# Kernel tuning notes

Hardware: AMD Instinct MI355X
Metric: run time of the kernel (lower is better)

The kernel has to match this reference:

```python
import jax, jax.numpy as jnp
import numpy as np

N_NODES = 100_000
N_EDGES = 1_600_000
N_GRAPHS = 512
HID = 64
NUM_CLASSES = 100
VOCAB = 3100
ID_OFFSET = 1500
BN_EPS = 1e-5


def setup_inputs() -> dict:
    key = jax.random.key(0)
    ks = jax.random.split(key, 8)
    node_ids = jax.random.randint(ks[0], (N_NODES,), 0, 1600)
    edge_src = jax.random.randint(ks[1], (N_EDGES,), 0, N_NODES)
    edge_dst = jax.random.randint(ks[2], (N_EDGES,), 0, N_NODES)
    graph_ids = jnp.sort(jax.random.randint(ks[3], (N_NODES,), 0, N_GRAPHS))
    emb = jax.random.normal(ks[4], (VOCAB, HID), dtype=jnp.float32) * 0.02
    # 3 GIN layers x 3 MLP linear layers, all 64->64 since embedding_dim == hidden
    Ws = jax.random.normal(ks[5], (3, 3, HID, HID), dtype=jnp.float32) * 0.05
    bs = jnp.zeros((3, 3, HID), dtype=jnp.float32)
    bn_gamma = jnp.ones((3, HID), dtype=jnp.float32)
    bn_beta = jnp.zeros((3, HID), dtype=jnp.float32)
    eps = jnp.zeros((3,), dtype=jnp.float32)  # learn_eps=True, init 0
    W_out = jax.random.normal(ks[6], (3 * HID, NUM_CLASSES), dtype=jnp.float32) * 0.05
    b_out = jnp.zeros((NUM_CLASSES,), dtype=jnp.float32)
    return {"node_ids": node_ids, "edge_src": edge_src, "edge_dst": edge_dst,
            "graph_ids": graph_ids, "emb": emb, "Ws": Ws, "bs": bs,
            "bn_gamma": bn_gamma, "bn_beta": bn_beta, "eps": eps,
            "W_out": W_out, "b_out": b_out}


def reference(node_ids, edge_src, edge_dst, graph_ids, emb, Ws, bs,
              bn_gamma, bn_beta, eps, W_out, b_out):
    n = node_ids.shape[0]
    h = emb[node_ids + ID_OFFSET]  # [N, HID]
    pooled = []
    for l in range(3):  # GIN layers (fixed small count)
        # GINConv, sum aggregator: (1+eps)*h + sum over in-edges of h[src]
        agg = jax.ops.segment_sum(h[edge_src], edge_dst, num_segments=n)
        x = (1.0 + eps[l]) * h + agg
        for m in range(3):
            x = jax.nn.relu(x @ Ws[l, m] + bs[l, m])
        mean = x.mean(axis=0)
        var = x.var(axis=0)  # biased var, as torch BN uses for normalization
        x = (x - mean) * jax.lax.rsqrt(var + BN_EPS) * bn_gamma[l] + bn_beta[l]
        h = x
        # dgl.sum_nodes: per-graph segment sum
        pooled.append(jax.ops.segment_sum(h, graph_ids, num_segments=N_GRAPHS))
    graph_features = jnp.concatenate(pooled, axis=-1)  # [G, 3*HID]
    return graph_features @ W_out + b_out  # [G, NUM_CLASSES]
```

## Files before the change

kernel.cpp:

```cpp
#include <hip/hip_runtime.h>

#define N_NODES 100000
#define N_EDGES 1600000
#define N_GRAPHS 512
#define HID 64
#define NUM_CLASSES 100
#define ID_OFFSET 1500
#define BN_EPS 1e-5f
#define CAP 64
#define NBKT 256
#define BSHIFT 9
#define NUSED ((N_NODES + 511) >> 9)
#define BCAP 10240
#define CBLK 98
#define CHUNK 16384
#define WPBLK 5
#define EMBBLK ((N_NODES * 32 + 1023) / 1024)
#define ZWORDS (98304 + 3072 + 100000)
#define ZBLK ((ZWORDS + 1023) / 1024)
#define DUMMY_ROW 100000
#define SREP 8
#define SSTRIDE 384

typedef __attribute__((ext_vector_type(8))) short short8;
typedef __attribute__((ext_vector_type(4))) float floatx4;

__device__ __forceinline__ float b2f(unsigned short u) {
    return __builtin_bit_cast(float, ((unsigned)u) << 16);
}
__device__ __forceinline__ unsigned short f2b(float f) {
    unsigned x = __builtin_bit_cast(unsigned, f);
    x += 0x7FFFu + ((x >> 16) & 1u);
    return (unsigned short)(x >> 16);
}

#define XSH(row, qq) ((((((row) >> 4) << 7) + ((qq) << 4) + (((row) & 15) ^ (qq))) * 8))


__global__ __launch_bounds__(1024) void prep_kernel(const int* __restrict__ src,
                                                    const int* __restrict__ dst,
                                                    int* __restrict__ cursor,
                                                    int* __restrict__ rec,
                                                    const float* __restrict__ Ws,
                                                    unsigned short* __restrict__ whi,
                                                    unsigned short* __restrict__ wlo,
                                                    const int* __restrict__ node_ids,
                                                    const int* __restrict__ gid,
                                                    const float* __restrict__ emb,
                                                    unsigned short* __restrict__ h,
                                                    unsigned short* __restrict__ xin,
                                                    int* __restrict__ gs,
                                                    int* __restrict__ ge,
                                                    unsigned* __restrict__ zbase) {
    __shared__ int hist[NBKT];
    __shared__ int base_s[NBKT];
    int t = threadIdx.x;
    int blk = blockIdx.x;

    if (blk < CBLK) {
        if (blk == 0 && t < 32) {
            ((unsigned*)(h + (size_t)DUMMY_ROW * 64))[t] = 0u;
            ((unsigned*)(xin + (size_t)DUMMY_ROW * 64))[t] = 0u;
        }
        if (t < NBKT) hist[t] = 0;
        __syncthreads();
        int cb = blk * CHUNK;
        int d_[16], s_[16];
#pragma unroll
        for (int k = 0; k < 16; ++k) {
            int i = cb + k * 1024 + t;
            d_[k] = (i < N_EDGES) ? dst[i] : -1;
            s_[k] = (i < N_EDGES) ? src[i] : 0;
            if (d_[k] >= 0) atomicAdd(&hist[((unsigned)d_[k] >> BSHIFT) & (NBKT - 1)], 1);
        }
        __syncthreads();
        if (t < NBKT) base_s[t] = (hist[t] > 0) ? atomicAdd(&cursor[t], hist[t]) : 0;
        __syncthreads();
        if (t < NBKT) hist[t] = 0;
        __syncthreads();
#pragma unroll
        for (int k = 0; k < 16; ++k) {
            if (d_[k] >= 0) {
                unsigned d = (unsigned)d_[k];
                int b = (d >> BSHIFT) & (NBKT - 1);
                int p = atomicAdd(&hist[b], 1);
                int g = base_s[b] + p;
                if ((unsigned)g < BCAP)
                    rec[b * BCAP + g] = ((int)(d & 511) << 17) | (s_[k] & 0x1FFFF);
            }
        }
    } else if (blk < CBLK + WPBLK) {
        int G = (blk - CBLK) * 1024 + t;
        if (G < 3 * 1536) {
            int l = G / 1536, Gp = G % 1536;
            int mm = Gp >> 9, rem = Gp & 511;
            int kq = rem >> 6, n = rem & 63;
            const float* Wp = Ws + l * 12288 + mm * 4096 + (kq * 8) * 64 + n;
            unsigned short uh[8], ul[8];
#pragma unroll
            for (int j = 0; j < 8; ++j) {
                float w = Wp[j * 64];
                unsigned short hi = f2b(w);
                uh[j] = hi;
                ul[j] = f2b(w - b2f(hi));
            }
            size_t off = (size_t)l * 12288 + (mm << 12) + XSH(n, kq);
            *(short8*)&whi[off] = *(short8*)uh;
            *(short8*)&wlo[off] = *(short8*)ul;
        }
    } else if (blk < CBLK + WPBLK + EMBBLK) {
        int idx = (blk - CBLK - WPBLK) * 1024 + t;
        if (idx < N_NODES * 32) {
            int n = idx >> 5, cp = idx & 31;
            const float2 e = *(const float2*)(emb + (((size_t)(node_ids[n] + ID_OFFSET)) << 6) + cp * 2);
            unsigned v = (unsigned)f2b(e.x) | ((unsigned)f2b(e.y) << 16);
            ((unsigned*)h)[n * 32 + cp] = v;
            if (cp == 0) {
                int g = gid[n] & (N_GRAPHS - 1);
                if (n == 0 || (gid[n - 1] & (N_GRAPHS - 1)) != g) gs[g] = n;
                if (n == N_NODES - 1 || (gid[n + 1] & (N_GRAPHS - 1)) != g) ge[g] = n + 1;
            }
        }
    } else {
        int idx = (blk - CBLK - WPBLK - EMBBLK) * 1024 + t;
        if (idx < ZWORDS) zbase[idx] = 0u;
    }
}


__global__ __launch_bounds__(1024) void fill_kernel(const int* __restrict__ rec,
                                                    const int* __restrict__ cursor,
                                                    int* __restrict__ cnt,
                                                    int* __restrict__ srcs) {
    __shared__ int lcnt[512];
    int t = threadIdx.x;
    int b = blockIdx.x;
    if (t < 512) lcnt[t] = 0;
    __syncthreads();
    int nb = cursor[b];
    if (nb < 0) nb = 0;
    if (nb > BCAP) nb = BCAP;
    const int* seg = rec + b * BCAP;
    for (int i = t; i < nb; i += 1024) {
        unsigned r = (unsigned)seg[i];
        int dl = (int)((r >> 17) & 511);
        int s = (int)(r & 0x1FFFF);
        int node = (b << BSHIFT) + dl;
        int p = atomicAdd(&lcnt[dl], 1);
        if (p < CAP && node < N_NODES) srcs[(node << 6) + p] = s;
    }
    __syncthreads();
    if (t < 512) {
        int node = (b << BSHIFT) + t;
        if (node < N_NODES) cnt[node] = lcnt[t];
    }
    __syncthreads();
    for (int i = t; i < 512 * 64; i += 1024) {
        int nl = i >> 6, p = i & 63;
        int node = (b << BSHIFT) + nl;
        if (node < N_NODES) {
            int deg = lcnt[nl];
            int degc = deg > CAP ? CAP : deg;
            int degp = (degc + 15) & ~15;
            if (degp < 16) degp = 16;
            if (p >= degc && p < degp) srcs[(node << 6) + p] = DUMMY_ROW;
        }
    }
}


__global__ __launch_bounds__(256) void agg_kernel(const unsigned short* __restrict__ x,
                                                  const int* __restrict__ cnt,
                                                  const int* __restrict__ srcs,
                                                  const float* __restrict__ eps, int l,
                                                  const float* __restrict__ stats,
                                                  const float* __restrict__ gamma,
                                                  const float* __restrict__ beta,
                                                  unsigned short* __restrict__ out) {
    int nb = __builtin_amdgcn_readfirstlane(((blockIdx.x << 2) + (threadIdx.x >> 6)) << 2);
    int lane = threadIdx.x & 63;
    int half = lane >> 5;
    int cl = lane & 31;
    const unsigned* __restrict__ xu = (const unsigned*)x;

    float scale = 1.0f + eps[l];
    float a0f = 1.0f, a1f = 1.0f, b0f = 0.0f, b1f = 0.0f;
    if (l > 0) {
        int lp = l - 1;
        float sm0 = 0.f, sm1 = 0.f, sq0 = 0.f, sq1 = 0.f;
#pragma unroll
        for (int rp = 0; rp < SREP; ++rp) {
            const float* sp = stats + rp * SSTRIDE + lp * 128;
            float2 a_ = *(const float2*)&sp[2 * cl];
            float2 b_ = *(const float2*)&sp[64 + 2 * cl];
            sm0 += a_.x; sm1 += a_.y;
            sq0 += b_.x; sq1 += b_.y;
        }
        float2 gm = *(const float2*)&gamma[lp * 64 + 2 * cl];
        float2 bt = *(const float2*)&beta[lp * 64 + 2 * cl];
        float mean0 = sm0 * (1.0f / N_NODES);
        float var0 = sq0 * (1.0f / N_NODES) - mean0 * mean0;
        float r0 = rsqrtf(var0 + BN_EPS);
        a0f = gm.x * r0;
        b0f = bt.x - mean0 * a0f;
        float mean1 = sm1 * (1.0f / N_NODES);
        float var1 = sq1 * (1.0f / N_NODES) - mean1 * mean1;
        float r1 = rsqrtf(var1 + BN_EPS);
        a1f = gm.y * r1;
        b1f = bt.y - mean1 * a1f;
    }

    int deg[4], degp[4];
    const int* row[4];
#pragma unroll
    for (int n = 0; n < 4; ++n) {
        int d = cnt[nb + n];
        int dc = d < 0 ? 0 : (d > CAP ? CAP : d);
        deg[n] = dc;
        int dp = (dc + 15) & ~15;
        degp[n] = dp < 16 ? 16 : dp;
        row[n] = srcs + ((size_t)(nb + n) << 6);
    }
    int cmax = degp[0];
    cmax = degp[1] > cmax ? degp[1] : cmax;
    cmax = degp[2] > cmax ? degp[2] : cmax;
    cmax = degp[3] > cmax ? degp[3] : cmax;

    unsigned us[4];
#pragma unroll
    for (int n = 0; n < 4; ++n) us[n] = xu[(size_t)(nb + n) * 32 + cl];

    float A0[4] = {0.f, 0.f, 0.f, 0.f}, A1[4] = {0.f, 0.f, 0.f, 0.f};
    float B0[4] = {0.f, 0.f, 0.f, 0.f}, B1[4] = {0.f, 0.f, 0.f, 0.f};

    {
        unsigned uv[4][8];
#pragma unroll
        for (int n = 0; n < 4; ++n)
#pragma unroll
            for (int k = 0; k < 8; ++k) {
                int ia = row[n][2 * k] & 0x1FFFF;
                int ib = row[n][2 * k + 1] & 0x1FFFF;
                int idx = half ? ib : ia;
                uv[n][k] = xu[(size_t)idx * 32 + cl];
            }
#pragma unroll
        for (int n = 0; n < 4; ++n)
#pragma unroll
            for (int k = 0; k < 8; ++k) {
                float lo = b2f((unsigned short)(uv[n][k] & 0xFFFF));
                float hi = b2f((unsigned short)(uv[n][k] >> 16));
                if (k & 1) { B0[n] += lo; B1[n] += hi; }
                else       { A0[n] += lo; A1[n] += hi; }
            }
    }

    for (int c = 16; c < cmax; c += 16) {
        unsigned uc[4][8];
#pragma unroll
        for (int n = 0; n < 4; ++n)
            if (c < degp[n])
#pragma unroll
                for (int k = 0; k < 8; ++k) {
                    int ia = row[n][c + 2 * k] & 0x1FFFF;
                    int ib = row[n][c + 2 * k + 1] & 0x1FFFF;
                    int idx = half ? ib : ia;
                    uc[n][k] = xu[(size_t)idx * 32 + cl];
                }
#pragma unroll
        for (int n = 0; n < 4; ++n)
            if (c < degp[n])
#pragma unroll
                for (int k = 0; k < 8; ++k) {
                    float lo = b2f((unsigned short)(uc[n][k] & 0xFFFF));
                    float hi = b2f((unsigned short)(uc[n][k] >> 16));
                    if (k & 1) { B0[n] += lo; B1[n] += hi; }
                    else       { A0[n] += lo; A1[n] += hi; }
                }
    }

#pragma unroll
    for (int n = 0; n < 4; ++n) {
        float S0 = (A0[n] + B0[n]);
        float S1 = (A1[n] + B1[n]);
        S0 += __shfl_xor(S0, 32);
        S1 += __shfl_xor(S1, 32);
        if (half == 0) {
            float selflo = b2f((unsigned short)(us[n] & 0xFFFF));
            float selfhi = b2f((unsigned short)(us[n] >> 16));
            float db = scale + (float)deg[n];
            float v0 = fmaf(a0f, fmaf(scale, selflo, S0), db * b0f);
            float v1 = fmaf(a1f, fmaf(scale, selfhi, S1), db * b1f);
            ((unsigned*)out)[(size_t)(nb + n) * 32 + cl] =
                (unsigned)f2b(v0) | ((unsigned)f2b(v1) << 16);
        }
    }
}


__global__ __launch_bounds__(256, 4) void mlp_kernel(unsigned short* __restrict__ x,
                                                     const unsigned short* __restrict__ whi,
                                                     const unsigned short* __restrict__ wlo,
                                                     const float* __restrict__ bs, int l,
                                                     float* __restrict__ stats,
                                                     const int* __restrict__ graph_ids,
                                                     float* __restrict__ pooled, int last) {
    __shared__ __align__(16) unsigned short xs[64 * 64];
    __shared__ int garr[64];
    __shared__ float ssum[256], sqq[256];
    int t = threadIdx.x;
    int nodebase = blockIdx.x * 64;
    int lane = t & 63, w = t >> 6;
    int m = lane & 15, q = lane >> 4;

    const unsigned short* xrow = x + (((size_t)(nodebase + w * 16 + m)) << 6);
    short8 a0[2];
#pragma unroll
    for (int kc = 0; kc < 2; ++kc)
        a0[kc] = *(const short8*)&xrow[kc * 32 + q * 8];

    if (lane < 16) {
        int n = nodebase + w * 16 + lane;
        garr[w * 16 + lane] = (n < N_NODES) ? (graph_ids[n] & (N_GRAPHS - 1)) : -1;
    }

    const float* bb = bs + l * 3 * 64;
    const unsigned short* whil = whi + (size_t)l * 12288;
    const unsigned short* wlol = wlo + (size_t)l * 12288;
    for (int mm = 0; mm < 3; ++mm) {
        short8 bl[2][4];
#pragma unroll
        for (int kc = 0; kc < 2; ++kc)
#pragma unroll
            for (int tj = 0; tj < 4; ++tj)
                bl[kc][tj] = *(const short8*)&wlol[(mm << 12) + XSH(tj * 16 + m, kc * 4 + q)];
        short8 a[2];
        if (mm == 0) {
#pragma unroll
            for (int kc = 0; kc < 2; ++kc) a[kc] = a0[kc];
        } else {
#pragma unroll
            for (int kc = 0; kc < 2; ++kc)
                a[kc] = *(const short8*)&xs[XSH(w * 16 + m, kc * 4 + q)];
        }

        floatx4 acc[4];
#pragma unroll
        for (int tj = 0; tj < 4; ++tj) {
            float bv = bb[mm * 64 + tj * 16 + m];
            acc[tj] = (floatx4){bv, bv, bv, bv};
        }
#pragma unroll
        for (int kc = 0; kc < 2; ++kc) {
            short8 bh[4];
#pragma unroll
            for (int tj = 0; tj < 4; ++tj)
                bh[tj] = *(const short8*)&whil[(mm << 12) + XSH(tj * 16 + m, kc * 4 + q)];
#pragma unroll
            for (int tj = 0; tj < 4; ++tj)
                acc[tj] = __builtin_amdgcn_mfma_f32_16x16x32_bf16(a[kc], bh[tj], acc[tj], 0, 0, 0);
        }
#pragma unroll
        for (int kc = 0; kc < 2; ++kc)
#pragma unroll
            for (int tj = 0; tj < 4; ++tj)
                acc[tj] = __builtin_amdgcn_mfma_f32_16x16x32_bf16(a[kc], bl[kc][tj], acc[tj], 0, 0, 0);
#pragma unroll
        for (int tj = 0; tj < 4; ++tj) {
            int col = tj * 16 + m;
#pragma unroll
            for (int r = 0; r < 4; ++r) {
                int row = w * 16 + q * 4 + r;
                float v = acc[tj][r];
                xs[XSH(row, col >> 3) + (col & 7)] = f2b(v > 0.f ? v : 0.f);
            }
        }
    }

    if (!last) {
        unsigned* xo = (unsigned*)x;
#pragma unroll
        for (int it = 0; it < 8; ++it) {
            int row = w * 16 + (lane >> 5) + it * 2;
            int cp = lane & 31;
            int col = cp * 2;
            unsigned val = *(const unsigned*)&xs[XSH(row, col >> 3) + (col & 7)];
            int node = nodebase + row;
            if (node < N_NODES) xo[(size_t)node * 32 + cp] = val;
        }
    }
    {
        int c = lane;
        float s = 0.f, q2 = 0.f, acc2 = 0.f;
        int cur = -1;
#pragma unroll
        for (int k = 0; k < 16; ++k) {
            int row = w * 16 + k;
            int g = garr[row];
            if (g >= 0) {
                float v = b2f(xs[XSH(row, c >> 3) + (c & 7)]);
                s += v;
                q2 += v * v;
                if (g != cur) {
                    if (cur >= 0) atomicAdd(&pooled[cur * 192 + l * 64 + c], acc2);
                    acc2 = 0.f;
                    cur = g;
                }
                acc2 += v;
            }
        }
        if (cur >= 0) atomicAdd(&pooled[cur * 192 + l * 64 + c], acc2);
        ssum[t] = s;
        sqq[t] = q2;
    }
    __syncthreads();
    if (t < 64) {
        float S = ssum[t] + ssum[t + 64] + ssum[t + 128] + ssum[t + 192];
        float Q = sqq[t] + sqq[t + 64] + sqq[t + 128] + sqq[t + 192];
        float* sp = stats + (blockIdx.x & (SREP - 1)) * SSTRIDE + l * 128;
        atomicAdd(&sp[t], S);
        atomicAdd(&sp[64 + t], Q);
    }
}


__global__ __launch_bounds__(256) void out_kernel(const float* __restrict__ pooled,
                                                  const float* __restrict__ stats,
                                                  const float* __restrict__ gamma,
                                                  const float* __restrict__ beta,
                                                  const int* __restrict__ gs,
                                                  const int* __restrict__ ge,
                                                  const float* __restrict__ Wo,
                                                  const float* __restrict__ bo,
                                                  float* __restrict__ out) {
    __shared__ float sab[384];
    int t = threadIdx.x;
    if (t < 192) {
        int l2 = t / 64, c = t & 63;
        float S = 0.f, Q = 0.f;
#pragma unroll
        for (int rp = 0; rp < SREP; ++rp) {
            S += stats[rp * SSTRIDE + l2 * 128 + c];
            Q += stats[rp * SSTRIDE + l2 * 128 + 64 + c];
        }
        float mean = S * (1.0f / N_NODES);
        float var = Q * (1.0f / N_NODES) - mean * mean;
        float rstd = rsqrtf(var + BN_EPS);
        float a = gamma[l2 * 64 + c] * rstd;
        sab[l2 * 128 + c] = a;
        sab[l2 * 128 + 64 + c] = beta[l2 * 64 + c] - mean * a;
    }
    __syncthreads();
    int idx = blockIdx.x * blockDim.x + t;
    if (idx < N_GRAPHS * NUM_CLASSES) {
        int g = idx / NUM_CLASSES, k = idx % NUM_CLASSES;
        float cg = (float)(ge[g] - gs[g]);
        float acc = bo[k];
        for (int l2 = 0; l2 < 3; ++l2)
            for (int c = 0; c < 64; ++c) {
                float gf = fmaf(sab[l2 * 128 + c], pooled[g * 192 + l2 * 64 + c],
                                sab[l2 * 128 + 64 + c] * cg);
                acc = fmaf(gf, Wo[(l2 * 64 + c) * NUM_CLASSES + k], acc);
            }
        out[idx] = acc;
    }
}

extern "C" void kernel_launch(void* const* d_in, const int* in_sizes, int n_in,
                              void* d_out, int out_size, void* d_ws, size_t ws_size,
                              hipStream_t stream) {
    const int*   node_ids  = (const int*)d_in[0];
    const int*   edge_src  = (const int*)d_in[1];
    const int*   edge_dst  = (const int*)d_in[2];
    const int*   graph_ids = (const int*)d_in[3];
    const float* emb       = (const float*)d_in[4];
    const float* Ws        = (const float*)d_in[5];
    const float* bs        = (const float*)d_in[6];
    const float* gamma     = (const float*)d_in[7];
    const float* beta      = (const float*)d_in[8];
    const float* eps       = (const float*)d_in[9];
    const float* W_out     = (const float*)d_in[10];
    const float* b_out     = (const float*)d_in[11];
    float* out = (float*)d_out;

    unsigned short* h    = (unsigned short*)d_ws;
    unsigned short* xin  = h + 6400000 + 8192;
    unsigned short* whi  = xin + 6400000 + 8192;
    unsigned short* wlo  = whi + 36864;
    int*   srcs   = (int*)(wlo + 36864);
    int*   rec    = srcs + 6400000;
    float* pooled = (float*)(rec + NUSED * BCAP);
    float* stats  = pooled + 98304;
    int*   cnt    = (int*)(stats + SREP * SSTRIDE);
    int*   gs     = cnt + 100000;
    int*   ge     = gs + 512;
    int*   cursor = ge + 512;

    hipMemsetAsync(gs, 0, (size_t)(512 + 512 + 256) * 4, stream);

    prep_kernel<<<CBLK + WPBLK + EMBBLK + ZBLK, 1024, 0, stream>>>(
        edge_src, edge_dst, cursor, rec, Ws, whi, wlo,
        node_ids, graph_ids, emb, h, xin, gs, ge, (unsigned*)pooled);
    fill_kernel<<<NUSED, 1024, 0, stream>>>(rec, cursor, cnt, srcs);

    const int MLP_BLK = (N_NODES + 63) / 64;
    const int AGG_BLK = N_NODES / 16;
    for (int l = 0; l < 3; ++l) {
        unsigned short* X = (l % 2 == 0) ? h : xin;
        unsigned short* A = (l % 2 == 0) ? xin : h;
        agg_kernel<<<AGG_BLK, 256, 0, stream>>>(X, cnt, srcs, eps, l, stats, gamma, beta, A);
        mlp_kernel<<<MLP_BLK, 256, 0, stream>>>(A, whi, wlo, bs, l, stats, graph_ids, pooled, l == 2);
    }

    out_kernel<<<(N_GRAPHS * NUM_CLASSES + 255) / 256, 256, 0, stream>>>(
        pooled, stats, gamma, beta, gs, ge, W_out, b_out, out);
}
```

Baseline: 298.5 us.

## Split MLP block into two waves over output columns for 16-node tiles

The MLP kernel now processes 16 nodes per 128-thread block, with each of two wavefronts computing half of the 64 output columns, instead of each wave owning 16 rows of a 64-node block. Ping-pong shared buffers plus a __syncthreads per linear layer let waves exchange the intermediate activations. The aim is more, smaller blocks for better latency hiding and fewer weight registers per wave. In exchange each wave reloads the same A fragments, syncs three extra times, and issues more stats/pool atomics per node because there are four times as many blocks.

```diff
diff --git a/kernel.cpp b/kernel.cpp
--- a/kernel.cpp
+++ b/kernel.cpp
@@ -298,42 +298,44 @@
 }
 
 
-__global__ __launch_bounds__(256, 4) void mlp_kernel(unsigned short* __restrict__ x,
+__global__ __launch_bounds__(128, 5) void mlp_kernel(unsigned short* __restrict__ x,
                                                      const unsigned short* __restrict__ whi,
                                                      const unsigned short* __restrict__ wlo,
                                                      const float* __restrict__ bs, int l,
                                                      float* __restrict__ stats,
                                                      const int* __restrict__ graph_ids,
                                                      float* __restrict__ pooled, int last) {
-    __shared__ __align__(16) unsigned short xs[64 * 64];
-    __shared__ int garr[64];
-    __shared__ float ssum[256], sqq[256];
+    __shared__ __align__(16) unsigned short xs[2 * 16 * 64];
+    __shared__ int garr[16];
+    __shared__ float ssum[128], sqq[128];
     int t = threadIdx.x;
-    int nodebase = blockIdx.x * 64;
+    int nodebase = blockIdx.x * 16;
     int lane = t & 63, w = t >> 6;
     int m = lane & 15, q = lane >> 4;
-
-    const unsigned short* xrow = x + (((size_t)(nodebase + w * 16 + m)) << 6);
+    int tjb = w * 2;
+
+    const unsigned short* xrow = x + (((size_t)(nodebase + m)) << 6);
     short8 a0[2];
 #pragma unroll
     for (int kc = 0; kc < 2; ++kc)
         a0[kc] = *(const short8*)&xrow[kc * 32 + q * 8];
 
-    if (lane < 16) {
-        int n = nodebase + w * 16 + lane;
-        garr[w * 16 + lane] = (n < N_NODES) ? (graph_ids[n] & (N_GRAPHS - 1)) : -1;
-    }
+    if (t < 16) garr[t] = graph_ids[nodebase + t] & (N_GRAPHS - 1);
 
     const float* bb = bs + l * 3 * 64;
     const unsigned short* whil = whi + (size_t)l * 12288;
     const unsigned short* wlol = wlo + (size_t)l * 12288;
+
     for (int mm = 0; mm < 3; ++mm) {
-        short8 bl[2][4];
+        unsigned short* xw = xs + ((mm & 1) ^ (mm == 0 ? 1 : 0) ? 1024 : 0);
+        xw = xs + ((mm == 1) ? 1024 : 0);
+        const unsigned short* xr = xs + ((mm == 2) ? 1024 : 0);
+        short8 bl[2][2];
 #pragma unroll
         for (int kc = 0; kc < 2; ++kc)
 #pragma unroll
-            for (int tj = 0; tj < 4; ++tj)
-                bl[kc][tj] = *(const short8*)&wlol[(mm << 12) + XSH(tj * 16 + m, kc * 4 + q)];
+            for (int j = 0; j < 2; ++j)
+                bl[kc][j] = *(const short8*)&wlol[(mm << 12) + XSH((tjb + j) * 16 + m, kc * 4 + q)];
         short8 a[2];
         if (mm == 0) {
 #pragma unroll
@@ -341,73 +343,74 @@
         } else {
 #pragma unroll
             for (int kc = 0; kc < 2; ++kc)
-                a[kc] = *(const short8*)&xs[XSH(w * 16 + m, kc * 4 + q)];
-        }
-
-        floatx4 acc[4];
-#pragma unroll
-        for (int tj = 0; tj < 4; ++tj) {
-            float bv = bb[mm * 64 + tj * 16 + m];
-            acc[tj] = (floatx4){bv, bv, bv, bv};
+                a[kc] = *(const short8*)&xr[XSH(m, kc * 4 + q)];
+        }
+
+        floatx4 acc[2];
+#pragma unroll
+        for (int j = 0; j < 2; ++j) {
+            float bv = bb[mm * 64 + (tjb + j) * 16 + m];
+            acc[j] = (floatx4){bv, bv, bv, bv};
         }
 #pragma unroll
         for (int kc = 0; kc < 2; ++kc) {
-            short8 bh[4];
-#pragma unroll
-            for (int tj = 0; tj < 4; ++tj)
-                bh[tj] = *(const short8*)&whil[(mm << 12) + XSH(tj * 16 + m, kc * 4 + q)];
-#pragma unroll
-            for (int tj = 0; tj < 4; ++tj)
-                acc[tj] = __builtin_amdgcn_mfma_f32_16x16x32_bf16(a[kc], bh[tj], acc[tj], 0, 0, 0);
+            short8 bh[2];
+#pragma unroll
+            for (int j = 0; j < 2; ++j)
+                bh[j] = *(const short8*)&whil[(mm << 12) + XSH((tjb + j) * 16 + m, kc * 4 + q)];
+#pragma unroll
+            for (int j = 0; j < 2; ++j)
+                acc[j] = __builtin_amdgcn_mfma_f32_16x16x32_bf16(a[kc], bh[j], acc[j], 0, 0, 0);
         }
 #pragma unroll
         for (int kc = 0; kc < 2; ++kc)
 #pragma unroll
-            for (int tj = 0; tj < 4; ++tj)
-                acc[tj] = __builtin_amdgcn_mfma_f32_16x16x32_bf16(a[kc], bl[kc][tj], acc[tj], 0, 0, 0);
-#pragma unroll
-        for (int tj = 0; tj < 4; ++tj) {
-            int col = tj * 16 + m;
+            for (int j = 0; j < 2; ++j)
+                acc[j] = __builtin_amdgcn_mfma_f32_16x16x32_bf16(a[kc], bl[kc][j], acc[j], 0, 0, 0);
+#pragma unroll
+        for (int j = 0; j < 2; ++j) {
+            int col = (tjb + j) * 16 + m;
 #pragma unroll
             for (int r = 0; r < 4; ++r) {
-                int row = w * 16 + q * 4 + r;
-                float v = acc[tj][r];
-                xs[XSH(row, col >> 3) + (col & 7)] = f2b(v > 0.f ? v : 0.f);
-            }
-        }
-    }
+                int row = q * 4 + r;
+                float v = acc[j][r];
+                xw[XSH(row, col >> 3) + (col & 7)] = f2b(v > 0.f ? v : 0.f);
+            }
+        }
+        __syncthreads();
+    }
+
+    const unsigned short* xf = xs;
 
     if (!last) {
         unsigned* xo = (unsigned*)x;
 #pragma unroll
-        for (int it = 0; it < 8; ++it) {
-            int row = w * 16 + (lane >> 5) + it * 2;
-            int cp = lane & 31;
+        for (int it = 0; it < 4; ++it) {
+            int row = (t >> 5) + it * 4;
+            int cp = t & 31;
             int col = cp * 2;
-            unsigned val = *(const unsigned*)&xs[XSH(row, col >> 3) + (col & 7)];
-            int node = nodebase + row;
-            if (node < N_NODES) xo[(size_t)node * 32 + cp] = val;
+            unsigned val = *(const unsigned*)&xf[XSH(row, col >> 3) + (col & 7)];
+            xo[(size_t)(nodebase + row) * 32 + cp] = val;
         }
     }
     {
-        int c = lane;
+        int c = t & 63;
+        int rh = t >> 6;
         float s = 0.f, q2 = 0.f, acc2 = 0.f;
         int cur = -1;
 #pragma unroll
-        for (int k = 0; k < 16; ++k) {
-            int row = w * 16 + k;
+        for (int k = 0; k < 8; ++k) {
+            int row = rh * 8 + k;
             int g = garr[row];
-            if (g >= 0) {
-                float v = b2f(xs[XSH(row, c >> 3) + (c & 7)]);
-                s += v;
-                q2 += v * v;
-                if (g != cur) {
-                    if (cur >= 0) atomicAdd(&pooled[cur * 192 + l * 64 + c], acc2);
-                    acc2 = 0.f;
-                    cur = g;
-                }
-                acc2 += v;
-            }
+            float v = b2f(xf[XSH(row, c >> 3) + (c & 7)]);
+            s += v;
+            q2 += v * v;
+            if (g != cur) {
+                if (cur >= 0) atomicAdd(&pooled[cur * 192 + l * 64 + c], acc2);
+                acc2 = 0.f;
+                cur = g;
+            }
+            acc2 += v;
         }
         if (cur >= 0) atomicAdd(&pooled[cur * 192 + l * 64 + c], acc2);
         ssum[t] = s;
@@ -415,8 +418,8 @@
     }
     __syncthreads();
     if (t < 64) {
-        float S = ssum[t] + ssum[t + 64] + ssum[t + 128] + ssum[t + 192];
-        float Q = sqq[t] + sqq[t + 64] + sqq[t + 128] + sqq[t + 192];
+        float S = ssum[t] + ssum[t + 64];
+        float Q = sqq[t] + sqq[t + 64];
         float* sp = stats + (blockIdx.x & (SREP - 1)) * SSTRIDE + l * 128;
         atomicAdd(&sp[t], S);
         atomicAdd(&sp[64 + t], Q);
@@ -503,13 +506,13 @@
         node_ids, graph_ids, emb, h, xin, gs, ge, (unsigned*)pooled);
     fill_kernel<<<NUSED, 1024, 0, stream>>>(rec, cursor, cnt, srcs);
 
-    const int MLP_BLK = (N_NODES + 63) / 64;
+    const int MLP_BLK = N_NODES / 16;
     const int AGG_BLK = N_NODES / 16;
     for (int l = 0; l < 3; ++l) {
         unsigned short* X = (l % 2 == 0) ? h : xin;
         unsigned short* A = (l % 2 == 0) ? xin : h;
         agg_kernel<<<AGG_BLK, 256, 0, stream>>>(X, cnt, srcs, eps, l, stats, gamma, beta, A);
-        mlp_kernel<<<MLP_BLK, 256, 0, stream>>>(A, whi, wlo, bs, l, stats, graph_ids, pooled, l == 2);
+        mlp_kernel<<<MLP_BLK, 128, 0, stream>>>(A, whi, wlo, bs, l, stats, graph_ids, pooled, l == 2);
     }
 
     out_kernel<<<(N_GRAPHS * NUM_CLASSES + 255) / 256, 256, 0, stream>>>(
```

Result: slower. 330.9 us (+10.9%).
